# Performance work log

Hardware: AMD Instinct MI355X
Metric: run time of the kernel (lower is better)

## Reference

```python
import jax, jax.numpy as jnp
import numpy as np

# Model dims (match init_kwargs)
B, L, D = 1, 2048, 1024
DI = 2048          # D_inner
N = 16             # SSM state size
DR = 64            # delta_rank
K = 4              # conv_1d_size
EPS = 1e-5
DELTA_MIN, DELTA_MAX, DELTA_FLOOR = 1e-3, 1e-1, 1e-4


def setup_inputs() -> dict:
    key = jax.random.key(0)
    ks = jax.random.split(key, 9)
    g = lambda i, shape, scale: (jax.random.normal(ks[i], shape, jnp.float32) * scale)
    x = g(0, (B, L, D), 1.0)
    rms_w = jnp.ones((D,), jnp.float32)
    in_proj_w = g(1, (D, 2 * DI), D ** -0.5)           # Linear D -> 2*DI, no bias
    conv_w = g(2, (DI, K), 0.3)                         # depthwise conv kernel
    conv_b = g(3, (DI,), 0.1)
    bcd_w = g(4, (DI, 2 * N + DR), DI ** -0.5)          # to_BCdelta, no bias
    dup_w = g(5, (DR, DI), DR ** -0.5)                  # delta_upscale weight
    # delta_upscale bias: inverse-softplus of log-uniform samples in [delta_min, delta_max]
    u = jax.random.uniform(ks[6], (DI,), jnp.float32)
    samples = jnp.clip(jnp.exp(u * (np.log(DELTA_MAX) - np.log(DELTA_MIN)) + np.log(DELTA_MIN)), DELTA_FLOOR)
    dup_b = samples + jnp.log(-jnp.expm1(-samples))
    # log(-A) with A = -[1..N] repeated over channels (S4D-real init)
    log_minus_A = jnp.tile(jnp.log(jnp.arange(1, N + 1, dtype=jnp.float32))[None, :], (DI, 1))
    D_param = jnp.ones((DI,), jnp.float32)              # skip parameter D
    out_proj_w = g(7, (DI, D), DI ** -0.5)              # Linear DI -> D, no bias
    return {"x": x, "rms_w": rms_w, "in_proj_w": in_proj_w, "conv_w": conv_w,
            "conv_b": conv_b, "bcd_w": bcd_w, "dup_w": dup_w, "dup_b": dup_b,
            "log_minus_A": log_minus_A, "D_param": D_param, "out_proj_w": out_proj_w}


def reference(x, rms_w, in_proj_w, conv_w, conv_b, bcd_w, dup_w, dup_b,
              log_minus_A, D_param, out_proj_w):
    b, l, _ = x.shape
    # RMSNorm
    xn = x * jax.lax.rsqrt(jnp.mean(x * x, axis=-1, keepdims=True) + EPS) * rms_w
    # in_proj and split into ssm branch / gating residual branch
    proj = xn @ in_proj_w                                  # (b,l,2*DI)
    xs, res = proj[..., :DI], proj[..., DI:]
    # causal depthwise conv1d (torch pads K-1 both sides then truncates -> left-pad only)
    xp = jnp.pad(xs, ((0, 0), (K - 1, 0), (0, 0)))         # (b,l+K-1,DI)
    conv = sum(xp[:, k:k + l, :] * conv_w[:, k] for k in range(K)) + conv_b
    xc = jax.nn.silu(conv)                                 # (b,l,DI)
    # S6 block
    bcd = xc @ bcd_w                                       # (b,l,DR+2N)
    delta_lr = bcd[..., :DR]
    Bm = bcd[..., DR:DR + N]                               # (b,l,N)
    Cm = bcd[..., DR + N:]                                 # (b,l,N)
    delta = jax.nn.softplus(delta_lr @ dup_w + dup_b)      # (b,l,DI)
    A = -jnp.exp(log_minus_A)                              # (DI,N)
    A_bar = jnp.exp(jnp.einsum('bld,dn->bldn', delta, A))  # (b,l,DI,N)
    B_bar_x = jnp.einsum('bld,bln,bld->bldn', delta, Bm, xc)
    # sequential selective scan: h_t = A_bar_t * h_{t-1} + B_bar_x_t
    def step(h, ab_bx):
        ab, bx = ab_bx
        h = ab * h + bx
        return h, h
    h0 = jnp.zeros((b, DI, N), x.dtype)
    _, hs = jax.lax.scan(step, h0, (jnp.swapaxes(A_bar, 0, 1), jnp.swapaxes(B_bar_x, 0, 1)))
    # hs: (l,b,DI,N); project out with C and add skip D
    y = jnp.einsum('bln,lbdn->bld', Cm, hs) + xc * D_param
    # gate, out_proj, residual
    y = y * jax.nn.silu(res)
    return y @ out_proj_w + x
```

## Files before the change

kernel.cpp:

```cpp
#include <hip/hip_runtime.h>
#include <hip/hip_bf16.h>
#include <math.h>

#define Lseq 2048
#define Dmod 1024
#define DI   2048
#define Nst  16
#define DRr  64
#define NCHUNK 32
#define LCHUNK 64
#define SPLITK 16
#define OSPLIT 4

typedef unsigned short u16;
typedef float  f32x4  __attribute__((ext_vector_type(4)));
typedef short  short8 __attribute__((ext_vector_type(8)));

__device__ __forceinline__ float sigmoidf_(float x) { return 1.f / (1.f + expf(-x)); }
__device__ __forceinline__ float softplusf_(float x) {
    return fmaxf(x, 0.f) + log1pf(expf(-fabsf(x)));
}
__device__ __forceinline__ u16 f2bf(float x) {
    union { float f; unsigned u; } v; v.f = x;
    unsigned r = (v.u + 0x7fffu + ((v.u >> 16) & 1u)) >> 16;
    return (u16)r;
}
__device__ __forceinline__ float bf2f(u16 h) {
    union { unsigned u; float f; } v; v.u = ((unsigned)h) << 16; return v.f;
}
__device__ __forceinline__ void async16(const void* g, void* l) {
    __builtin_amdgcn_global_load_lds((__attribute__((address_space(1))) void*)g,
                                     (__attribute__((address_space(3))) void*)l, 16, 0, 0);
}
template <int N> __device__ __forceinline__ void vmwait() {
    if constexpr (N == 0)      asm volatile("s_waitcnt vmcnt(0)" ::: "memory");
    else if constexpr (N == 6) asm volatile("s_waitcnt vmcnt(6)" ::: "memory");
    else if constexpr (N == 7) asm volatile("s_waitcnt vmcnt(7)" ::: "memory");
    else                       asm volatile("s_waitcnt vmcnt(8)" ::: "memory");
}

struct __align__(8) u16x4 { u16 x, y, z, w; };

__device__ __forceinline__ void wsplit_body(const float* __restrict__ W, int R, int Cn,
                                            int bx, int by, float (*t)[33],
                                            u16* __restrict__ Th, u16* __restrict__ Tl) {
    int r0 = by * 32, c0 = bx * 32;
    int tr = threadIdx.x >> 3;
    int tc4 = (threadIdx.x & 7) * 4;
    float4 v = *reinterpret_cast<const float4*>(&W[(size_t)(r0 + tr) * Cn + c0 + tc4]);
    t[tr][tc4 + 0] = v.x; t[tr][tc4 + 1] = v.y;
    t[tr][tc4 + 2] = v.z; t[tr][tc4 + 3] = v.w;
    __syncthreads();
    u16x4 H, L;
    u16* hp = &H.x; u16* lp = &L.x;
    #pragma unroll
    for (int q = 0; q < 4; q++) {
        float xv = t[tc4 + q][tr];
        u16 h = f2bf(xv); hp[q] = h; lp[q] = f2bf(xv - bf2f(h));
    }
    size_t o = (size_t)(c0 + tr) * R + r0 + tc4;
    *reinterpret_cast<u16x4*>(&Th[o]) = H;
    *reinterpret_cast<u16x4*>(&Tl[o]) = L;
}

__global__ __launch_bounds__(256) void prep1_k(const float* __restrict__ x,
                                               const float* __restrict__ rms_w,
                                               u16* __restrict__ xnH, u16* __restrict__ xnL,
                                               const float* __restrict__ Wi,
                                               u16* __restrict__ WiH, u16* __restrict__ WiL) {
    __shared__ float t[32][33];
    __shared__ float s4[4];
    int b = blockIdx.x;
    if (b < 2048) {
        int row = b, tid = threadIdx.x;
        float4 v = reinterpret_cast<const float4*>(x + (size_t)row * Dmod)[tid];
        float ss = v.x * v.x + v.y * v.y + v.z * v.z + v.w * v.w;
        #pragma unroll
        for (int m = 32; m >= 1; m >>= 1) ss += __shfl_xor(ss, m);
        if ((tid & 63) == 0) s4[tid >> 6] = ss;
        __syncthreads();
        float tot = s4[0] + s4[1] + s4[2] + s4[3];
        float scale = rsqrtf(tot * (1.0f / Dmod) + 1e-5f);
        float4 wv = reinterpret_cast<const float4*>(rms_w)[tid];
        float o[4] = {v.x * scale * wv.x, v.y * scale * wv.y,
                      v.z * scale * wv.z, v.w * scale * wv.w};
        u16x4 H, L;
        u16* hp = &H.x; u16* lp = &L.x;
        #pragma unroll
        for (int q = 0; q < 4; q++) {
            u16 h = f2bf(o[q]); hp[q] = h; lp[q] = f2bf(o[q] - bf2f(h));
        }
        reinterpret_cast<u16x4*>(xnH + (size_t)row * Dmod)[tid] = H;
        reinterpret_cast<u16x4*>(xnL + (size_t)row * Dmod)[tid] = L;
    } else {
        int bb = b - 2048;
        wsplit_body(Wi, 1024, 4096, bb & 127, bb >> 7, t, WiH, WiL);
    }
}

__global__ __launch_bounds__(256) void wsplit3_k(const float* __restrict__ Wo,
                                                 const float* __restrict__ Wb,
                                                 const float* __restrict__ Wd,
                                                 u16* WoH, u16* WoL,
                                                 u16* bwTH, u16* bwTL,
                                                 u16* dwTH, u16* dwTL) {
    __shared__ float t[32][33];
    int b = blockIdx.x;
    if (b < 2048) {
        wsplit_body(Wo, 2048, 1024, b & 31, b >> 5, t, WoH, WoL);
    } else if (b < 2240) {
        int bb = b - 2048;
        wsplit_body(Wb, 2048, 96, bb % 3, bb / 3, t, bwTH, bwTL);
    } else {
        int bb = b - 2240;
        wsplit_body(Wd, 64, 2048, bb & 63, bb >> 6, t, dwTH, dwTL);
    }
}

template <int BM, int BN, int EPI>
__global__ __launch_bounds__(256) void gemm_mfma3(
    const u16* __restrict__ Ah, const u16* __restrict__ Al,
    const u16* __restrict__ Bh, const u16* __restrict__ Bl,
    float* __restrict__ C, float* __restrict__ C2, const float* __restrict__ aux,
    int M, int N, int K) {
    constexpr int BK = 32;
    constexpr int MF = BM / 32, NF = BN / 32;
    constexpr int CH_A = BM / 16, CH_B = BN / 16;
    constexpr int NLD = (2 * CH_A + 2 * CH_B) / 4;
    __shared__ u16 AhT[2][BM][BK], AlT[2][BM][BK], BhT[2][BN][BK], BlT[2][BN][BK];
    const int tid = threadIdx.x, lane = tid & 63, wid = tid >> 6;
    const int wr = wid >> 1, wc = wid & 1;
    const int lr = lane & 15;
    const int sw = (lane >> 1) & 3;
    const int lkq = ((lane >> 4) ^ sw) * 8;
    const int bm0 = blockIdx.y * BM, bn0 = blockIdx.x * BN;
    const int srow = lane >> 2;
    const int scol_ = ((lane & 3) ^ ((lane >> 3) & 3)) * 8;

    int kbeg = 0, kend = K;
    if (EPI == 5) {
        int ks = K / gridDim.z;
        kbeg = blockIdx.z * ks;
        kend = kbeg + ks;
    }
    const int nt = (kend - kbeg) / BK;

    auto STAGE = [&](int buf, int k0) {
        int ci = 0;
        #pragma unroll
        for (int c = 0; c < CH_A; c++, ci++) if ((ci & 3) == wid) {
            size_t g = (size_t)(bm0 + c * 16 + srow) * K + (k0 + scol_);
            async16(Ah + g, (u16*)&AhT[buf][0][0] + c * 512 + lane * 8);
        }
        #pragma unroll
        for (int c = 0; c < CH_A; c++, ci++) if ((ci & 3) == wid) {
            size_t g = (size_t)(bm0 + c * 16 + srow) * K + (k0 + scol_);
            async16(Al + g, (u16*)&AlT[buf][0][0] + c * 512 + lane * 8);
        }
        #pragma unroll
        for (int c = 0; c < CH_B; c++, ci++) if ((ci & 3) == wid) {
            size_t g = (size_t)(bn0 + c * 16 + srow) * K + (k0 + scol_);
            async16(Bh + g, (u16*)&BhT[buf][0][0] + c * 512 + lane * 8);
        }
        #pragma unroll
        for (int c = 0; c < CH_B; c++, ci++) if ((ci & 3) == wid) {
            size_t g = (size_t)(bn0 + c * 16 + srow) * K + (k0 + scol_);
            async16(Bl + g, (u16*)&BlT[buf][0][0] + c * 512 + lane * 8);
        }
    };

    f32x4 acc[MF][NF];
    #pragma unroll
    for (int i = 0; i < MF; i++)
        #pragma unroll
        for (int j = 0; j < NF; j++) acc[i][j] = (f32x4){0.f, 0.f, 0.f, 0.f};

    STAGE(0, kbeg);
    if (nt > 1) STAGE(1, kbeg + BK);

    for (int t = 0; t < nt; ++t) {
        const int cur = t & 1;
        if (t < nt - 1) vmwait<NLD>(); else vmwait<0>();
        __builtin_amdgcn_s_barrier();

        short8 ah[MF], al[MF], bh[NF], bl[NF];
        #pragma unroll
        for (int i = 0; i < MF; i++) {
            int r = wr * (MF * 16) + i * 16 + lr;
            ah[i] = *(const short8*)&AhT[cur][r][lkq];
            al[i] = *(const short8*)&AlT[cur][r][lkq];
        }
        #pragma unroll
        for (int j = 0; j < NF; j++) {
            int r = wc * (NF * 16) + j * 16 + lr;
            bh[j] = *(const short8*)&BhT[cur][r][lkq];
            bl[j] = *(const short8*)&BlT[cur][r][lkq];
        }
        asm volatile("s_waitcnt lgkmcnt(0)" ::: "memory");
        __builtin_amdgcn_sched_barrier(0);
        __builtin_amdgcn_s_barrier();
        if (t + 2 < nt) STAGE(cur, kbeg + (t + 2) * BK);

        __builtin_amdgcn_s_setprio(1);
        #pragma unroll
        for (int i = 0; i < MF; i++)
            #pragma unroll
            for (int j = 0; j < NF; j++) {
                acc[i][j] = __builtin_amdgcn_mfma_f32_16x16x32_bf16(ah[i], bh[j], acc[i][j], 0, 0, 0);
                acc[i][j] = __builtin_amdgcn_mfma_f32_16x16x32_bf16(ah[i], bl[j], acc[i][j], 0, 0, 0);
                acc[i][j] = __builtin_amdgcn_mfma_f32_16x16x32_bf16(al[i], bh[j], acc[i][j], 0, 0, 0);
            }
        __builtin_amdgcn_s_setprio(0);
    }

    float* Cp = C;
    if (EPI == 5) Cp = C + (size_t)blockIdx.z * M * N;
    #pragma unroll
    for (int i = 0; i < MF; i++)
        #pragma unroll
        for (int j = 0; j < NF; j++) {
            int rowg = bm0 + wr * (MF * 16) + i * 16 + (lane >> 4) * 4;
            int colg = bn0 + wc * (NF * 16) + j * 16 + lr;
            #pragma unroll
            for (int q = 0; q < 4; q++) {
                float v = acc[i][j][q];
                if (EPI == 5) {
                    Cp[(size_t)(rowg + q) * N + colg] = v;
                } else if (EPI == 2) {
                    C[(size_t)(rowg + q) * N + colg] = softplusf_(v + aux[colg]);
                } else if (EPI == 4) {
                    if (colg < DI) C[(size_t)(rowg + q) * DI + colg] = v;
                    else C2[(size_t)(rowg + q) * DI + (colg - DI)] = v * sigmoidf_(v);
                }
            }
        }
}

__global__ __launch_bounds__(256) void bcd_reduce_k(const float* __restrict__ partial,
                                                    float* __restrict__ bcd,
                                                    u16* __restrict__ bH,
                                                    u16* __restrict__ bL) {
    const int NT = Lseq * 96;
    int t = blockIdx.x * 256 + threadIdx.x;
    float s = 0.f;
    #pragma unroll
    for (int z = 0; z < SPLITK; z++) s += partial[(size_t)z * NT + t];
    bcd[t] = s;
    int col = t % 96, row = t / 96;
    if (col < DRr) {
        u16 h = f2bf(s);
        bH[(size_t)row * DRr + col] = h;
        bL[(size_t)row * DRr + col] = f2bf(s - bf2f(h));
    }
}

__global__ __launch_bounds__(256) void out_reduce_k(const float* __restrict__ part,
                                                    const float* __restrict__ x,
                                                    float* __restrict__ out) {
    int t = blockIdx.x * 256 + threadIdx.x;
    const size_t NT = (size_t)Lseq * Dmod;
    float4 xv = reinterpret_cast<const float4*>(x)[t];
    float4 o = xv;
    #pragma unroll
    for (int z = 0; z < OSPLIT; z++) {
        float4 p = reinterpret_cast<const float4*>(part + (size_t)z * NT)[t];
        o.x += p.x; o.y += p.y; o.z += p.z; o.w += p.w;
    }
    reinterpret_cast<float4*>(out)[t] = o;
}

__global__ __launch_bounds__(256) void conv_silu_k(const float* __restrict__ xs,
                                                   const float* __restrict__ cw,
                                                   const float* __restrict__ cb,
                                                   u16* __restrict__ xcH,
                                                   u16* __restrict__ xcL) {
    int d = blockIdx.x * 256 + threadIdx.x;
    int l0 = blockIdx.y * 32;
    float4 w = reinterpret_cast<const float4*>(cw)[d];
    float b = cb[d];
    float p0 = 0.f, p1 = 0.f, p2 = 0.f;
    if (l0 > 0) {
        p0 = xs[(size_t)(l0 - 3) * DI + d];
        p1 = xs[(size_t)(l0 - 2) * DI + d];
        p2 = xs[(size_t)(l0 - 1) * DI + d];
    }
    for (int l = l0; l < l0 + 32; ++l) {
        float c = xs[(size_t)l * DI + d];
        float s = b;
        s = fmaf(p0, w.x, s);
        s = fmaf(p1, w.y, s);
        s = fmaf(p2, w.z, s);
        s = fmaf(c,  w.w, s);
        float v = s * sigmoidf_(s);
        size_t o = (size_t)l * DI + d;
        u16 h = f2bf(v);
        xcH[o] = h;
        xcL[o] = f2bf(v - bf2f(h));
        p0 = p1; p1 = p2; p2 = c;
    }
}

__global__ __launch_bounds__(256) void scan1_k(const float* __restrict__ delta,
                                               const u16* __restrict__ xcH,
                                               const u16* __restrict__ xcL,
                                               const float* __restrict__ bcd,
                                               const float* __restrict__ lmA,
                                               float* __restrict__ Pb,
                                               float* __restrict__ Sb) {
    __shared__ float Bs[LCHUNK][16];
    const int tid = threadIdx.x;
    const int d = (blockIdx.x * 256 + tid) >> 1;
    const int half = tid & 1;
    const int c = blockIdx.y;
    const int l0 = c * LCHUNK;
    {
        int row = tid >> 2, q = (tid & 3) * 4;
        float4 v = *reinterpret_cast<const float4*>(&bcd[(size_t)(l0 + row) * 96 + DRr + q]);
        *reinterpret_cast<float4*>(&Bs[row][q]) = v;
    }
    __syncthreads();
    float negA[8], h[8];
    #pragma unroll
    for (int j = 0; j < 8; j++) {
        negA[j] = -__expf(lmA[(size_t)d * Nst + half * 8 + j]);
        h[j] = 0.f;
    }
    float sdv = 0.f;
    for (int l = 0; l < LCHUNK; ++l) {
        size_t o = (size_t)(l0 + l) * DI + d;
        float dv = delta[o];
        float xcv = bf2f(xcH[o]) + bf2f(xcL[o]);
        sdv += dv;
        float dvx = dv * xcv;
        #pragma unroll
        for (int j = 0; j < 8; j++) {
            float a = __expf(dv * negA[j]);
            h[j] = fmaf(a, h[j], dvx * Bs[l][half * 8 + j]);
        }
    }
    size_t base = ((size_t)c * DI + d) * Nst + half * 8;
    #pragma unroll
    for (int j = 0; j < 8; j++) {
        Pb[base + j] = __expf(sdv * negA[j]);
        Sb[base + j] = h[j];
    }
}

__global__ __launch_bounds__(256) void scan2_k(float* __restrict__ PH,
                                               const float* __restrict__ Sb) {
    int t = blockIdx.x * 256 + threadIdx.x;
    float H = 0.f;
    for (int c = 0; c < NCHUNK; c++) {
        size_t idx = (size_t)c * (DI * Nst) + t;
        float P = PH[idx], S = Sb[idx];
        PH[idx] = H;
        H = S + P * H;
    }
}

__global__ __launch_bounds__(256) void scan3_k(const float* __restrict__ delta,
                                               const u16* __restrict__ xcH,
                                               const u16* __restrict__ xcL,
                                               const float* __restrict__ bcd,
                                               const float* __restrict__ lmA,
                                               const float* __restrict__ Dp,
                                               const float* __restrict__ gate,
                                               const float* __restrict__ Hinit,
                                               u16* __restrict__ yH,
                                               u16* __restrict__ yL) {
    __shared__ float BCs[LCHUNK][32];
    const int tid = threadIdx.x;
    const int d = (blockIdx.x * 256 + tid) >> 1;
    const int half = tid & 1;
    const int c = blockIdx.y;
    const int l0 = c * LCHUNK;
    #pragma unroll
    for (int i = 0; i < 2; i++) {
        int idx = tid + 256 * i;
        int row = idx >> 3, q = (idx & 7) * 4;
        float4 v = *reinterpret_cast<const float4*>(&bcd[(size_t)(l0 + row) * 96 + DRr + q]);
        *reinterpret_cast<float4*>(&BCs[row][q]) = v;
    }
    __syncthreads();
    float negA[8], h[8];
    size_t hbase = ((size_t)c * DI + d) * Nst + half * 8;
    #pragma unroll
    for (int j = 0; j < 8; j++) {
        negA[j] = -__expf(lmA[(size_t)d * Nst + half * 8 + j]);
        h[j] = Hinit[hbase + j];
    }
    float Dpv = Dp[d];
    for (int l = 0; l < LCHUNK; ++l) {
        size_t o = (size_t)(l0 + l) * DI + d;
        float dv = delta[o];
        float xcv = bf2f(xcH[o]) + bf2f(xcL[o]);
        float dvx = dv * xcv;
        float yp = 0.f;
        #pragma unroll
        for (int j = 0; j < 8; j++) {
            float a = __expf(dv * negA[j]);
            h[j] = fmaf(a, h[j], dvx * BCs[l][half * 8 + j]);
            yp = fmaf(BCs[l][16 + half * 8 + j], h[j], yp);
        }
        yp += __shfl_xor(yp, 1);
        if (half == 0) {
            float yv = (yp + xcv * Dpv) * gate[o];
            u16 hq = f2bf(yv);
            yH[o] = hq;
            yL[o] = f2bf(yv - bf2f(hq));
        }
    }
}

extern "C" void kernel_launch(void* const* d_in, const int* in_sizes, int n_in,
                              void* d_out, int out_size, void* d_ws, size_t ws_size,
                              hipStream_t stream) {
    const float* x          = (const float*)d_in[0];
    const float* rms_w      = (const float*)d_in[1];
    const float* in_proj_w  = (const float*)d_in[2];
    const float* conv_w     = (const float*)d_in[3];
    const float* conv_b     = (const float*)d_in[4];
    const float* bcd_w      = (const float*)d_in[5];
    const float* dup_w      = (const float*)d_in[6];
    const float* dup_b      = (const float*)d_in[7];
    const float* lmA        = (const float*)d_in[8];
    const float* Dp         = (const float*)d_in[9];
    const float* out_proj_w = (const float*)d_in[10];
    float* out = (float*)d_out;
    char*  W   = (char*)d_ws;

    const size_t MB = 1ull << 20;
    u16*   WiH  = (u16*)(W + 0);
    u16*   WiL  = (u16*)(W + 8 * MB);
    float* delta= (float*)(W + 0);
    float* xs   = (float*)(W + 16 * MB);
    float* part = (float*)(W + 16 * MB);
    u16*   bwTH = (u16*)(W + 28 * MB);
    u16*   bwTL = (u16*)(W + 28 * MB + 384 * 1024);
    u16*   dwTH = (u16*)(W + 28 * MB + 768 * 1024);
    u16*   dwTL = (u16*)(W + 28 * MB + 1024 * 1024);
    u16*   bcdH = (u16*)(W + 28 * MB + 1280 * 1024);
    u16*   bcdL = (u16*)(W + 28 * MB + 1536 * 1024);
    float* Sb   = (float*)(W + 16 * MB);
    u16*   yH   = (u16*)(W + 16 * MB);
    u16*   yL   = (u16*)(W + 24 * MB);
    float* gate = (float*)(W + 32 * MB);
    u16*   xcH  = (u16*)(W + 48 * MB);
    u16*   xcL  = (u16*)(W + 56 * MB);
    float* opart= (float*)(W + 32 * MB);
    u16*   xnH  = (u16*)(W + 64 * MB);
    u16*   xnL  = (u16*)(W + 68 * MB);
    u16*   WoH  = (u16*)(W + 64 * MB);
    u16*   WoL  = (u16*)(W + 68 * MB);
    float* bcd  = (float*)(W + 72 * MB);
    float* Pb   = (float*)(W + 73 * MB);

    prep1_k<<<2048 + 4096, 256, 0, stream>>>(x, rms_w, xnH, xnL, in_proj_w, WiH, WiL);
    gemm_mfma3<128, 128, 4><<<dim3(4096 / 128, Lseq / 128), 256, 0, stream>>>(
        xnH, xnL, WiH, WiL, xs, gate, nullptr, Lseq, 2 * DI, Dmod);
    conv_silu_k<<<dim3(DI / 256, Lseq / 32), 256, 0, stream>>>(xs, conv_w, conv_b, xcH, xcL);
    wsplit3_k<<<2368, 256, 0, stream>>>(out_proj_w, bcd_w, dup_w,
                                        WoH, WoL, bwTH, bwTL, dwTH, dwTL);
    gemm_mfma3<128, 96, 5><<<dim3(1, Lseq / 128, SPLITK), 256, 0, stream>>>(
        xcH, xcL, bwTH, bwTL, part, nullptr, nullptr, Lseq, 96, DI);
    bcd_reduce_k<<<Lseq * 96 / 256, 256, 0, stream>>>(part, bcd, bcdH, bcdL);
    gemm_mfma3<64, 128, 2><<<dim3(DI / 128, Lseq / 64), 256, 0, stream>>>(
        bcdH, bcdL, dwTH, dwTL, delta, nullptr, dup_b, Lseq, DI, DRr);
    scan1_k<<<dim3(16, NCHUNK), 256, 0, stream>>>(delta, xcH, xcL, bcd, lmA, Pb, Sb);
    scan2_k<<<dim3(DI * Nst / 256), 256, 0, stream>>>(Pb, Sb);
    scan3_k<<<dim3(16, NCHUNK), 256, 0, stream>>>(delta, xcH, xcL, bcd, lmA, Dp, gate, Pb, yH, yL);
    gemm_mfma3<128, 128, 5><<<dim3(Dmod / 128, Lseq / 128, OSPLIT), 256, 0, stream>>>(
        yH, yL, WoH, WoL, opart, nullptr, nullptr, Lseq, Dmod, DI);
    out_reduce_k<<<Lseq * Dmod / 1024, 256, 0, stream>>>(opart, x, out);
}
```

Before: 238.2 us.

## Simplify GEMM pipeline to single-stage prefetch and store xs as split bf16

The GEMM main loop drops the two-tile-ahead prefetch with partial vmcnt waits. It now issues the next tile's loads at the start of each iteration and waits for all loads plus a barrier after the MFMAs. Separately, the in_proj epilogue writes the xs half as hi/lo bf16 pairs instead of fp32, and the conv kernel reconstructs values from them, which is meant to cut epilogue store and conv read traffic. The full vmcnt(0) wait each iteration may expose more load latency than the deeper pipeline did.

```diff
diff --git a/kernel.cpp b/kernel.cpp
--- a/kernel.cpp
+++ b/kernel.cpp
@@ -31,12 +31,6 @@
 __device__ __forceinline__ void async16(const void* g, void* l) {
     __builtin_amdgcn_global_load_lds((__attribute__((address_space(1))) void*)g,
                                      (__attribute__((address_space(3))) void*)l, 16, 0, 0);
-}
-template <int N> __device__ __forceinline__ void vmwait() {
-    if constexpr (N == 0)      asm volatile("s_waitcnt vmcnt(0)" ::: "memory");
-    else if constexpr (N == 6) asm volatile("s_waitcnt vmcnt(6)" ::: "memory");
-    else if constexpr (N == 7) asm volatile("s_waitcnt vmcnt(7)" ::: "memory");
-    else                       asm volatile("s_waitcnt vmcnt(8)" ::: "memory");
 }
 
 struct __align__(8) u16x4 { u16 x, y, z, w; };
@@ -121,12 +115,13 @@
 __global__ __launch_bounds__(256) void gemm_mfma3(
     const u16* __restrict__ Ah, const u16* __restrict__ Al,
     const u16* __restrict__ Bh, const u16* __restrict__ Bl,
-    float* __restrict__ C, float* __restrict__ C2, const float* __restrict__ aux,
+    float* __restrict__ C, float* __restrict__ C2,
+    u16* __restrict__ U1, u16* __restrict__ U2,
+    const float* __restrict__ aux,
     int M, int N, int K) {
     constexpr int BK = 32;
     constexpr int MF = BM / 32, NF = BN / 32;
     constexpr int CH_A = BM / 16, CH_B = BN / 16;
-    constexpr int NLD = (2 * CH_A + 2 * CH_B) / 4;
     __shared__ u16 AhT[2][BM][BK], AlT[2][BM][BK], BhT[2][BN][BK], BlT[2][BN][BK];
     const int tid = threadIdx.x, lane = tid & 63, wid = tid >> 6;
     const int wr = wid >> 1, wc = wid & 1;
@@ -176,12 +171,12 @@
         for (int j = 0; j < NF; j++) acc[i][j] = (f32x4){0.f, 0.f, 0.f, 0.f};
 
     STAGE(0, kbeg);
-    if (nt > 1) STAGE(1, kbeg + BK);
+    asm volatile("s_waitcnt vmcnt(0)" ::: "memory");
+    __builtin_amdgcn_s_barrier();
 
     for (int t = 0; t < nt; ++t) {
         const int cur = t & 1;
-        if (t < nt - 1) vmwait<NLD>(); else vmwait<0>();
-        __builtin_amdgcn_s_barrier();
+        if (t + 1 < nt) STAGE(cur ^ 1, kbeg + (t + 1) * BK);
 
         short8 ah[MF], al[MF], bh[NF], bl[NF];
         #pragma unroll
@@ -198,9 +193,6 @@
         }
         asm volatile("s_waitcnt lgkmcnt(0)" ::: "memory");
         __builtin_amdgcn_sched_barrier(0);
-        __builtin_amdgcn_s_barrier();
-        if (t + 2 < nt) STAGE(cur, kbeg + (t + 2) * BK);
-
         __builtin_amdgcn_s_setprio(1);
         #pragma unroll
         for (int i = 0; i < MF; i++)
@@ -211,6 +203,10 @@
                 acc[i][j] = __builtin_amdgcn_mfma_f32_16x16x32_bf16(al[i], bh[j], acc[i][j], 0, 0, 0);
             }
         __builtin_amdgcn_s_setprio(0);
+        if (t + 1 < nt) {
+            asm volatile("s_waitcnt vmcnt(0)" ::: "memory");
+            __builtin_amdgcn_s_barrier();
+        }
     }
 
     float* Cp = C;
@@ -229,8 +225,14 @@
                 } else if (EPI == 2) {
                     C[(size_t)(rowg + q) * N + colg] = softplusf_(v + aux[colg]);
                 } else if (EPI == 4) {
-                    if (colg < DI) C[(size_t)(rowg + q) * DI + colg] = v;
-                    else C2[(size_t)(rowg + q) * DI + (colg - DI)] = v * sigmoidf_(v);
+                    if (colg < DI) {
+                        size_t o = (size_t)(rowg + q) * DI + colg;
+                        u16 hh = f2bf(v);
+                        U1[o] = hh;
+                        U2[o] = f2bf(v - bf2f(hh));
+                    } else {
+                        C2[(size_t)(rowg + q) * DI + (colg - DI)] = v * sigmoidf_(v);
+                    }
                 }
             }
         }
@@ -269,7 +271,8 @@
     reinterpret_cast<float4*>(out)[t] = o;
 }
 
-__global__ __launch_bounds__(256) void conv_silu_k(const float* __restrict__ xs,
+__global__ __launch_bounds__(256) void conv_silu_k(const u16* __restrict__ xsH,
+                                                   const u16* __restrict__ xsL,
                                                    const float* __restrict__ cw,
                                                    const float* __restrict__ cb,
                                                    u16* __restrict__ xcH,
@@ -280,19 +283,22 @@
     float b = cb[d];
     float p0 = 0.f, p1 = 0.f, p2 = 0.f;
     if (l0 > 0) {
-        p0 = xs[(size_t)(l0 - 3) * DI + d];
-        p1 = xs[(size_t)(l0 - 2) * DI + d];
-        p2 = xs[(size_t)(l0 - 1) * DI + d];
+        size_t o0 = (size_t)(l0 - 3) * DI + d;
+        size_t o1 = (size_t)(l0 - 2) * DI + d;
+        size_t o2 = (size_t)(l0 - 1) * DI + d;
+        p0 = bf2f(xsH[o0]) + bf2f(xsL[o0]);
+        p1 = bf2f(xsH[o1]) + bf2f(xsL[o1]);
+        p2 = bf2f(xsH[o2]) + bf2f(xsL[o2]);
     }
     for (int l = l0; l < l0 + 32; ++l) {
-        float c = xs[(size_t)l * DI + d];
+        size_t o = (size_t)l * DI + d;
+        float c = bf2f(xsH[o]) + bf2f(xsL[o]);
         float s = b;
         s = fmaf(p0, w.x, s);
         s = fmaf(p1, w.y, s);
         s = fmaf(p2, w.z, s);
         s = fmaf(c,  w.w, s);
         float v = s * sigmoidf_(s);
-        size_t o = (size_t)l * DI + d;
         u16 h = f2bf(v);
         xcH[o] = h;
         xcL[o] = f2bf(v - bf2f(h));
@@ -433,7 +439,8 @@
     u16*   WiH  = (u16*)(W + 0);
     u16*   WiL  = (u16*)(W + 8 * MB);
     float* delta= (float*)(W + 0);
-    float* xs   = (float*)(W + 16 * MB);
+    u16*   xsH  = (u16*)(W + 16 * MB);
+    u16*   xsL  = (u16*)(W + 24 * MB);
     float* part = (float*)(W + 16 * MB);
     u16*   bwTH = (u16*)(W + 28 * MB);
     u16*   bwTL = (u16*)(W + 28 * MB + 384 * 1024);
@@ -457,19 +464,19 @@
 
     prep1_k<<<2048 + 4096, 256, 0, stream>>>(x, rms_w, xnH, xnL, in_proj_w, WiH, WiL);
     gemm_mfma3<128, 128, 4><<<dim3(4096 / 128, Lseq / 128), 256, 0, stream>>>(
-        xnH, xnL, WiH, WiL, xs, gate, nullptr, Lseq, 2 * DI, Dmod);
-    conv_silu_k<<<dim3(DI / 256, Lseq / 32), 256, 0, stream>>>(xs, conv_w, conv_b, xcH, xcL);
+        xnH, xnL, WiH, WiL, nullptr, gate, xsH, xsL, nullptr, Lseq, 2 * DI, Dmod);
+    conv_silu_k<<<dim3(DI / 256, Lseq / 32), 256, 0, stream>>>(xsH, xsL, conv_w, conv_b, xcH, xcL);
     wsplit3_k<<<2368, 256, 0, stream>>>(out_proj_w, bcd_w, dup_w,
                                         WoH, WoL, bwTH, bwTL, dwTH, dwTL);
     gemm_mfma3<128, 96, 5><<<dim3(1, Lseq / 128, SPLITK), 256, 0, stream>>>(
-        xcH, xcL, bwTH, bwTL, part, nullptr, nullptr, Lseq, 96, DI);
+        xcH, xcL, bwTH, bwTL, part, nullptr, nullptr, nullptr, nullptr, Lseq, 96, DI);
     bcd_reduce_k<<<Lseq * 96 / 256, 256, 0, stream>>>(part, bcd, bcdH, bcdL);
     gemm_mfma3<64, 128, 2><<<dim3(DI / 128, Lseq / 64), 256, 0, stream>>>(
-        bcdH, bcdL, dwTH, dwTL, delta, nullptr, dup_b, Lseq, DI, DRr);
+        bcdH, bcdL, dwTH, dwTL, delta, nullptr, nullptr, nullptr, dup_b, Lseq, DI, DRr);
     scan1_k<<<dim3(16, NCHUNK), 256, 0, stream>>>(delta, xcH, xcL, bcd, lmA, Pb, Sb);
     scan2_k<<<dim3(DI * Nst / 256), 256, 0, stream>>>(Pb, Sb);
     scan3_k<<<dim3(16, NCHUNK), 256, 0, stream>>>(delta, xcH, xcL, bcd, lmA, Dp, gate, Pb, yH, yL);
     gemm_mfma3<128, 128, 5><<<dim3(Dmod / 128, Lseq / 128, OSPLIT), 256, 0, stream>>>(
-        yH, yL, WoH, WoL, opart, nullptr, nullptr, Lseq, Dmod, DI);
+        yH, yL, WoH, WoL, opart, nullptr, nullptr, nullptr, nullptr, Lseq, Dmod, DI);
     out_reduce_k<<<Lseq * Dmod / 1024, 256, 0, stream>>>(opart, x, out);
 }
```

New measurement: 237.3 us. No clear change (-0.4%).
